# Kernel optimization log

Hardware: AMD Instinct MI355X
Metric: run time of the kernel (lower is better)

Reference implementation:

```python
import jax, jax.numpy as jnp
import numpy as np

N_NODES = 100000
N_EDGES = 1600000
D_IN = 128
D_HID = 128
N_CLS = 64
EPS = 1e-12  # torch F.normalize default eps


def setup_inputs() -> dict:
    key = jax.random.key(0)
    ks = jax.random.split(key, 8)
    x = jax.random.normal(ks[0], (N_NODES, D_IN), dtype=jnp.float32)
    src = jax.random.randint(ks[1], (N_EDGES,), 0, N_NODES, dtype=jnp.int32)
    dst = jax.random.randint(ks[2], (N_EDGES,), 0, N_NODES, dtype=jnp.int32)
    edge_weight = jax.random.uniform(ks[3], (N_EDGES,), dtype=jnp.float32)
    W1 = jax.random.normal(ks[4], (D_IN, D_HID), dtype=jnp.float32) * (1.0 / np.sqrt(D_IN))
    b1 = jnp.zeros((D_HID,), dtype=jnp.float32)
    W2 = jax.random.normal(ks[5], (D_HID, N_CLS), dtype=jnp.float32) * (1.0 / np.sqrt(D_HID))
    b2 = jnp.zeros((N_CLS,), dtype=jnp.float32)
    return {"x": x, "src": src, "dst": dst, "edge_weight": edge_weight,
            "W1": W1, "b1": b1, "W2": W2, "b2": b2}


def _spmm(h, src, dst, w):
    # sparse adjacency aggregation: out[i] = sum_{e: dst[e]==i} w[e] * h[src[e]]
    msgs = h[src] * w[:, None]  # [E, D] gather + scale
    return jax.ops.segment_sum(msgs, dst, num_segments=N_NODES)


def reference(x, src, dst, edge_weight, W1, b1, W2, b2):
    # F.normalize: row-wise L2 normalization
    norm = jnp.sqrt(jnp.sum(x * x, axis=1, keepdims=True))
    xn = x / jnp.maximum(norm, EPS)
    # GCN layer 1: A @ (X W1 + b1), ReLU (dropout is identity in eval)
    h = xn @ W1 + b1
    h = jax.nn.relu(_spmm(h, src, dst, edge_weight))
    # GCN layer 2: A @ (H W2 + b2)
    h2 = _spmm(h @ W2 + b2, src, dst, edge_weight)
    # final softmax over classes
    return jax.nn.softmax(h2, axis=-1)
```

## Files before the change

kernel.cpp:

```cpp
#include <hip/hip_runtime.h>
#include <math.h>

constexpr int NN = 100000;
constexpr int NE = 1600000;
constexpr int DI = 128;
constexpr int DH = 128;
constexpr int NC = 64;
constexpr int NB = (NN + 255) / 256;
constexpr int GB = 2048;
constexpr int HB = 1024;

__device__ __forceinline__ unsigned short f2bf(float f) {
    const unsigned u = __float_as_uint(f);
    return (unsigned short)((u + 0x7FFFu + ((u >> 16) & 1u)) >> 16);
}
__device__ __forceinline__ float bf_lo(unsigned u) {
    return __uint_as_float(u << 16);
}
__device__ __forceinline__ float bf_hi(unsigned u) {
    return __uint_as_float(u & 0xFFFF0000u);
}
constexpr float INV_WQ = 1.0f / 32767.0f;

__global__ __launch_bounds__(512, 4) void k_gemm1_hist(
    const float* __restrict__ x, const float* __restrict__ W1,
    const float* __restrict__ b1, unsigned short* __restrict__ z1h,
    const int* __restrict__ dst, int* __restrict__ cnt,
    int* __restrict__ rank)
{
    __shared__ float4 sWq[32 * 64];
    __shared__ float sx[8][2][DI];

    const int tid = threadIdx.x;
    const int bid = blockIdx.x;

    if (bid >= GB) {
        const int hb = bid - GB;
        for (int e = hb * 512 + tid; e < NE; e += HB * 512)
            rank[e] = atomicAdd(&cnt[dst[e]], 1);
        return;
    }

    const int c0 = (bid & 1) * 64;
    const int chunk = bid >> 1;
    for (int i = tid; i < 32 * 64; i += 512) {
        const int k4 = i >> 6, c = i & 63;
        const float* wp = W1 + (size_t)(4 * k4) * DH + c0 + c;
        sWq[i] = make_float4(wp[0], wp[DH], wp[2 * DH], wp[3 * DH]);
    }
    __syncthreads();

    const int wave = tid >> 6, lane = tid & 63;
    const float bias = b1[c0 + lane];

    for (int base = (chunk * 8 + wave) * 2; base < NN; base += 16384) {
        #pragma unroll
        for (int r = 0; r < 2; ++r) {
            const int row = base + r;
            float a0 = 0.f, a1 = 0.f;
            if (row < NN) {
                a0 = x[(size_t)row * DI + lane];
                a1 = x[(size_t)row * DI + 64 + lane];
            }
            float ss = a0 * a0 + a1 * a1;
            #pragma unroll
            for (int off = 32; off; off >>= 1) ss += __shfl_xor(ss, off);
            const float rinv = 1.0f / fmaxf(sqrtf(ss), 1e-12f);
            sx[wave][r][lane]      = a0 * rinv;
            sx[wave][r][64 + lane] = a1 * rinv;
        }

        float acc0 = bias, acc1 = bias;
        #pragma unroll 4
        for (int k4 = 0; k4 < 32; ++k4) {
            const float4 w  = sWq[k4 * 64 + lane];
            const float4 xa = *(const float4*)(&sx[wave][0][4 * k4]);
            const float4 xb = *(const float4*)(&sx[wave][1][4 * k4]);
            acc0 = fmaf(xa.x, w.x, acc0); acc0 = fmaf(xa.y, w.y, acc0);
            acc0 = fmaf(xa.z, w.z, acc0); acc0 = fmaf(xa.w, w.w, acc0);
            acc1 = fmaf(xb.x, w.x, acc1); acc1 = fmaf(xb.y, w.y, acc1);
            acc1 = fmaf(xb.z, w.z, acc1); acc1 = fmaf(xb.w, w.w, acc1);
        }
        if (base < NN)
            z1h[(size_t)base * DH + c0 + lane] = f2bf(acc0);
        if (base + 1 < NN)
            z1h[(size_t)(base + 1) * DH + c0 + lane] = f2bf(acc1);
    }
}

__global__ __launch_bounds__(256) void k_packW2q(
    const float* __restrict__ W2, float4* __restrict__ W2q)
{
    const int i = blockIdx.x * 256 + threadIdx.x;
    const int k4 = i >> 6, c = i & 63;
    W2q[i] = make_float4(W2[(size_t)(4 * k4 + 0) * NC + c],
                         W2[(size_t)(4 * k4 + 1) * NC + c],
                         W2[(size_t)(4 * k4 + 2) * NC + c],
                         W2[(size_t)(4 * k4 + 3) * NC + c]);
}

__global__ __launch_bounds__(256) void k_scanA(
    const int* __restrict__ cnt, int* __restrict__ rowptr,
    int* __restrict__ bsum)
{
    __shared__ int tmp[256];
    const int t = threadIdx.x;
    const int gid = blockIdx.x * 256 + t;
    const int v = (gid < NN) ? cnt[gid] : 0;
    tmp[t] = v;
    __syncthreads();
    #pragma unroll
    for (int off = 1; off < 256; off <<= 1) {
        const int add = (t >= off) ? tmp[t - off] : 0;
        __syncthreads();
        tmp[t] += add;
        __syncthreads();
    }
    if (gid < NN) rowptr[gid] = tmp[t] - v;
    if (t == 255) bsum[blockIdx.x] = tmp[255];
}

__global__ __launch_bounds__(512) void k_scanB(int* __restrict__ bsum)
{
    __shared__ int tmp[512];
    const int t = threadIdx.x;
    const int v = (t < NB) ? bsum[t] : 0;
    tmp[t] = v;
    __syncthreads();
    #pragma unroll
    for (int off = 1; off < 512; off <<= 1) {
        const int add = (t >= off) ? tmp[t - off] : 0;
        __syncthreads();
        tmp[t] += add;
        __syncthreads();
    }
    if (t < NB) bsum[t] = tmp[t] - v;
}

__global__ __launch_bounds__(256) void k_scanC(
    int* __restrict__ rowptr, const int* __restrict__ bsum)
{
    const int gid = blockIdx.x * 256 + threadIdx.x;
    if (gid < NN) rowptr[gid] += bsum[blockIdx.x];
    if (gid == 0) rowptr[NN] = NE;
}

__global__ __launch_bounds__(256) void k_scatter(
    const int* __restrict__ src, const int* __restrict__ dst,
    const float* __restrict__ ew, const int* __restrict__ rowptr,
    const int* __restrict__ rank, unsigned* __restrict__ srcw)
{
    for (int e = blockIdx.x * 256 + threadIdx.x; e < NE; e += gridDim.x * 256) {
        const int pos = rowptr[dst[e]] + rank[e];
        const unsigned wq = (unsigned)__float2int_rn(ew[e] * 32767.f);
        srcw[pos] = (((unsigned)src[e]) << 15) | wq;
    }
}

__global__ __launch_bounds__(512, 4) void k_spmm1_gemm2(
    const unsigned short* __restrict__ h, const int* __restrict__ rowptr,
    const unsigned* __restrict__ srcw, const float4* __restrict__ W2q,
    const float* __restrict__ b2, unsigned short* __restrict__ z2h)
{
    __shared__ float4 sW2q[32 * 64];
    __shared__ float sagg[8][DH];

    const int tid = threadIdx.x;
    #pragma unroll
    for (int i = 0; i < 4; ++i)
        sW2q[tid + i * 512] = W2q[tid + i * 512];
    __syncthreads();

    const int wave = tid >> 6, lane = tid & 63;
    const float bias = b2[lane];
    const unsigned* hu = (const unsigned*)h;

    for (int row = blockIdx.x * 8 + wave; row < NN; row += gridDim.x * 8) {
        const int start = rowptr[row], end = rowptr[row + 1];
        float acc0 = 0.f, acc1 = 0.f;
        int e = start;
        for (; e + 16 <= end; e += 16) {
            unsigned p[16], u[16];
            #pragma unroll
            for (int j = 0; j < 16; ++j) p[j] = srcw[e + j];
            #pragma unroll
            for (int j = 0; j < 16; ++j) u[j] = hu[((p[j] >> 15) << 6) | lane];
            #pragma unroll
            for (int j = 0; j < 16; ++j) {
                const float w = (float)(p[j] & 0x7FFFu) * INV_WQ;
                acc0 = fmaf(w, bf_lo(u[j]), acc0);
                acc1 = fmaf(w, bf_hi(u[j]), acc1);
            }
        }
        for (; e + 8 <= end; e += 8) {
            unsigned p[8], u[8];
            #pragma unroll
            for (int j = 0; j < 8; ++j) p[j] = srcw[e + j];
            #pragma unroll
            for (int j = 0; j < 8; ++j) u[j] = hu[((p[j] >> 15) << 6) | lane];
            #pragma unroll
            for (int j = 0; j < 8; ++j) {
                const float w = (float)(p[j] & 0x7FFFu) * INV_WQ;
                acc0 = fmaf(w, bf_lo(u[j]), acc0);
                acc1 = fmaf(w, bf_hi(u[j]), acc1);
            }
        }
        for (; e < end; ++e) {
            const unsigned p = srcw[e];
            const unsigned u = hu[((p >> 15) << 6) | lane];
            const float w = (float)(p & 0x7FFFu) * INV_WQ;
            acc0 = fmaf(w, bf_lo(u), acc0);
            acc1 = fmaf(w, bf_hi(u), acc1);
        }
        *(float2*)&sagg[wave][2 * lane] =
            make_float2(fmaxf(acc0, 0.f), fmaxf(acc1, 0.f));

        float acc = bias;
        #pragma unroll 4
        for (int k4 = 0; k4 < 32; ++k4) {
            const float4 w = sW2q[k4 * 64 + lane];
            const float4 a = *(const float4*)(&sagg[wave][4 * k4]);
            acc = fmaf(a.x, w.x, acc);
            acc = fmaf(a.y, w.y, acc);
            acc = fmaf(a.z, w.z, acc);
            acc = fmaf(a.w, w.w, acc);
        }
        z2h[(size_t)row * NC + lane] = f2bf(acc);
    }
}

__global__ __launch_bounds__(256, 8) void k_spmm2_softmax(
    const unsigned short* __restrict__ z2h, const int* __restrict__ rowptr,
    const unsigned* __restrict__ srcw, float* __restrict__ out)
{
    const int row = blockIdx.x * 4 + (threadIdx.x >> 6);
    if (row >= NN) return;
    const int lane = threadIdx.x & 63;
    const int start = rowptr[row], end = rowptr[row + 1];
    float acc = 0.f;
    int e = start;
    for (; e + 16 <= end; e += 16) {
        unsigned p[16]; unsigned short t[16];
        #pragma unroll
        for (int j = 0; j < 16; ++j) p[j] = srcw[e + j];
        #pragma unroll
        for (int j = 0; j < 16; ++j) t[j] = z2h[((p[j] >> 15) << 6) | lane];
        #pragma unroll
        for (int j = 0; j < 16; ++j)
            acc = fmaf((float)(p[j] & 0x7FFFu) * INV_WQ,
                       __uint_as_float((unsigned)t[j] << 16), acc);
    }
    for (; e + 8 <= end; e += 8) {
        unsigned p[8]; unsigned short t[8];
        #pragma unroll
        for (int j = 0; j < 8; ++j) p[j] = srcw[e + j];
        #pragma unroll
        for (int j = 0; j < 8; ++j) t[j] = z2h[((p[j] >> 15) << 6) | lane];
        #pragma unroll
        for (int j = 0; j < 8; ++j)
            acc = fmaf((float)(p[j] & 0x7FFFu) * INV_WQ,
                       __uint_as_float((unsigned)t[j] << 16), acc);
    }
    for (; e < end; ++e) {
        const unsigned p = srcw[e];
        const float v = __uint_as_float(
            (unsigned)z2h[((p >> 15) << 6) | lane] << 16);
        acc = fmaf((float)(p & 0x7FFFu) * INV_WQ, v, acc);
    }
    float m = acc;
    #pragma unroll
    for (int off = 32; off; off >>= 1) m = fmaxf(m, __shfl_xor(m, off));
    const float ex = __expf(acc - m);
    float s = ex;
    #pragma unroll
    for (int off = 32; off; off >>= 1) s += __shfl_xor(s, off);
    out[(size_t)row * NC + lane] = ex / s;
}

extern "C" void kernel_launch(void* const* d_in, const int* in_sizes, int n_in,
                              void* d_out, int out_size, void* d_ws,
                              size_t ws_size, hipStream_t stream)
{
    const float* x  = (const float*)d_in[0];
    const int* src  = (const int*)d_in[1];
    const int* dst  = (const int*)d_in[2];
    const float* ew = (const float*)d_in[3];
    const float* W1 = (const float*)d_in[4];
    const float* b1 = (const float*)d_in[5];
    const float* W2 = (const float*)d_in[6];
    const float* b2 = (const float*)d_in[7];
    float* out = (float*)d_out;

    char* base = (char*)d_ws;
    unsigned short* z1h = (unsigned short*)base;  base += (size_t)NN * DH * 2;
    unsigned short* z2h = (unsigned short*)base;  base += (size_t)NN * NC * 2;
    unsigned* srcw = (unsigned*)base;             base += (size_t)NE * 4;
    int* rank   = (int*)base;                     base += (size_t)NE * 4;
    int* rowptr = (int*)base;                     base += ((size_t)NN + 2) * 4;
    int* cnt    = (int*)base;                     base += (size_t)NN * 4;
    int* bsum   = (int*)base;                     base += 512 * 4;
    float4* W2q = (float4*)base;                  base += 2048 * 16;

    hipMemsetAsync(cnt, 0, (size_t)NN * 4, stream);

    k_packW2q<<<8, 256, 0, stream>>>(W2, W2q);
    k_gemm1_hist<<<GB + HB, 512, 0, stream>>>(x, W1, b1, z1h, dst, cnt, rank);

    k_scanA  <<<NB, 256, 0, stream>>>(cnt, rowptr, bsum);
    k_scanB  <<<1, 512, 0, stream>>>(bsum);
    k_scanC  <<<NB, 256, 0, stream>>>(rowptr, bsum);
    k_scatter<<<2048, 256, 0, stream>>>(src, dst, ew, rowptr, rank, srcw);

    k_spmm1_gemm2   <<<2048, 512, 0, stream>>>(z1h, rowptr, srcw, W2q, b2, z2h);
    k_spmm2_softmax <<<(NN + 3) / 4, 256, 0, stream>>>(z2h, rowptr, srcw, out);
}
```

Measured before the change: 353.4 us.

## Split fused GEMM1/histogram kernel and widen GEMM1 register tile to 4 rows x 2 columns

Separates the degree histogram (atomic rank assignment) from the normalize+GEMM1 kernel into its own launch. The GEMM1 kernel now has each wave compute 4 rows and both 64-column halves, with W1 packed as interleaved float4 pairs, so each LDS weight load feeds more FMAs and the row normalization is no longer duplicated across two column blocks. The cost is an extra kernel launch and the loss of overlap between the atomic histogram and the GEMM work.

```diff
diff --git a/kernel.cpp b/kernel.cpp
--- a/kernel.cpp
+++ b/kernel.cpp
@@ -7,8 +7,6 @@
 constexpr int DH = 128;
 constexpr int NC = 64;
 constexpr int NB = (NN + 255) / 256;
-constexpr int GB = 2048;
-constexpr int HB = 1024;
 
 __device__ __forceinline__ unsigned short f2bf(float f) {
     const unsigned u = __float_as_uint(f);
@@ -22,40 +20,29 @@
 }
 constexpr float INV_WQ = 1.0f / 32767.0f;
 
-__global__ __launch_bounds__(512, 4) void k_gemm1_hist(
+__global__ __launch_bounds__(512) void k_norm_gemm1(
     const float* __restrict__ x, const float* __restrict__ W1,
-    const float* __restrict__ b1, unsigned short* __restrict__ z1h,
-    const int* __restrict__ dst, int* __restrict__ cnt,
-    int* __restrict__ rank)
-{
-    __shared__ float4 sWq[32 * 64];
-    __shared__ float sx[8][2][DI];
+    const float* __restrict__ b1, unsigned short* __restrict__ z1h)
+{
+    __shared__ float4 sW4[64][64];
+    __shared__ float sx[8][4][DI];
 
     const int tid = threadIdx.x;
-    const int bid = blockIdx.x;
-
-    if (bid >= GB) {
-        const int hb = bid - GB;
-        for (int e = hb * 512 + tid; e < NE; e += HB * 512)
-            rank[e] = atomicAdd(&cnt[dst[e]], 1);
-        return;
-    }
-
-    const int c0 = (bid & 1) * 64;
-    const int chunk = bid >> 1;
-    for (int i = tid; i < 32 * 64; i += 512) {
-        const int k4 = i >> 6, c = i & 63;
-        const float* wp = W1 + (size_t)(4 * k4) * DH + c0 + c;
-        sWq[i] = make_float4(wp[0], wp[DH], wp[2 * DH], wp[3 * DH]);
+    for (int i = tid; i < 64 * 64; i += 512) {
+        const int k2 = i >> 6, c = i & 63;
+        const float* wp = W1 + (size_t)(2 * k2) * DH + c;
+        sW4[k2][c] = make_float4(wp[0], wp[64], wp[DH], wp[DH + 64]);
     }
     __syncthreads();
 
     const int wave = tid >> 6, lane = tid & 63;
-    const float bias = b1[c0 + lane];
-
-    for (int base = (chunk * 8 + wave) * 2; base < NN; base += 16384) {
-        #pragma unroll
-        for (int r = 0; r < 2; ++r) {
+    const float bias0 = b1[lane];
+    const float bias1 = b1[64 + lane];
+
+    for (int base = (blockIdx.x * 8 + wave) * 4; base < NN;
+         base += gridDim.x * 32) {
+        #pragma unroll
+        for (int r = 0; r < 4; ++r) {
             const int row = base + r;
             float a0 = 0.f, a1 = 0.f;
             if (row < NN) {
@@ -70,21 +57,35 @@
             sx[wave][r][64 + lane] = a1 * rinv;
         }
 
-        float acc0 = bias, acc1 = bias;
-        #pragma unroll 4
-        for (int k4 = 0; k4 < 32; ++k4) {
-            const float4 w  = sWq[k4 * 64 + lane];
-            const float4 xa = *(const float4*)(&sx[wave][0][4 * k4]);
-            const float4 xb = *(const float4*)(&sx[wave][1][4 * k4]);
-            acc0 = fmaf(xa.x, w.x, acc0); acc0 = fmaf(xa.y, w.y, acc0);
-            acc0 = fmaf(xa.z, w.z, acc0); acc0 = fmaf(xa.w, w.w, acc0);
-            acc1 = fmaf(xb.x, w.x, acc1); acc1 = fmaf(xb.y, w.y, acc1);
-            acc1 = fmaf(xb.z, w.z, acc1); acc1 = fmaf(xb.w, w.w, acc1);
-        }
-        if (base < NN)
-            z1h[(size_t)base * DH + c0 + lane] = f2bf(acc0);
-        if (base + 1 < NN)
-            z1h[(size_t)(base + 1) * DH + c0 + lane] = f2bf(acc1);
+        float acc[4][2];
+        #pragma unroll
+        for (int r = 0; r < 4; ++r) { acc[r][0] = bias0; acc[r][1] = bias1; }
+
+        #pragma unroll 2
+        for (int k2 = 0; k2 < 64; k2 += 2) {
+            const float4 w0 = sW4[k2][lane];
+            const float4 w1 = sW4[k2 + 1][lane];
+            #pragma unroll
+            for (int r = 0; r < 4; ++r) {
+                const float4 xv = *(const float4*)(&sx[wave][r][2 * k2]);
+                acc[r][0] = fmaf(xv.x, w0.x, acc[r][0]);
+                acc[r][1] = fmaf(xv.x, w0.y, acc[r][1]);
+                acc[r][0] = fmaf(xv.y, w0.z, acc[r][0]);
+                acc[r][1] = fmaf(xv.y, w0.w, acc[r][1]);
+                acc[r][0] = fmaf(xv.z, w1.x, acc[r][0]);
+                acc[r][1] = fmaf(xv.z, w1.y, acc[r][1]);
+                acc[r][0] = fmaf(xv.w, w1.z, acc[r][0]);
+                acc[r][1] = fmaf(xv.w, w1.w, acc[r][1]);
+            }
+        }
+        #pragma unroll
+        for (int r = 0; r < 4; ++r) {
+            const int row = base + r;
+            if (row < NN) {
+                z1h[(size_t)row * DH + lane]      = f2bf(acc[r][0]);
+                z1h[(size_t)row * DH + 64 + lane] = f2bf(acc[r][1]);
+            }
+        }
     }
 }
 
@@ -97,6 +98,14 @@
                          W2[(size_t)(4 * k4 + 1) * NC + c],
                          W2[(size_t)(4 * k4 + 2) * NC + c],
                          W2[(size_t)(4 * k4 + 3) * NC + c]);
+}
+
+__global__ __launch_bounds__(256) void k_hist(
+    const int* __restrict__ dst, int* __restrict__ cnt,
+    int* __restrict__ rank)
+{
+    for (int e = blockIdx.x * 256 + threadIdx.x; e < NE; e += gridDim.x * 256)
+        rank[e] = atomicAdd(&cnt[dst[e]], 1);
 }
 
 __global__ __launch_bounds__(256) void k_scanA(
@@ -304,8 +313,9 @@
     hipMemsetAsync(cnt, 0, (size_t)NN * 4, stream);
 
     k_packW2q<<<8, 256, 0, stream>>>(W2, W2q);
-    k_gemm1_hist<<<GB + HB, 512, 0, stream>>>(x, W1, b1, z1h, dst, cnt, rank);
-
+    k_norm_gemm1<<<1024, 512, 0, stream>>>(x, W1, b1, z1h);
+
+    k_hist   <<<2048, 256, 0, stream>>>(dst, cnt, rank);
     k_scanA  <<<NB, 256, 0, stream>>>(cnt, rowptr, bsum);
     k_scanB  <<<1, 512, 0, stream>>>(bsum);
     k_scanC  <<<NB, 256, 0, stream>>>(rowptr, bsum);
```

After: 333.3 us. -5.7%, faster.
